# Kernel optimization log

Hardware: AMD Instinct MI355X
Metric: run time of the kernel (lower is better)

## Reference

```python
import jax, jax.numpy as jnp
import numpy as np

# tag2index constants
PAD, START, END, T = 0, 14, 15, 16
B, L, V, E, H = 128, 512, 30000, 256, 256


def _lstm(xs, w_ih, w_hh, b, reverse=False):
    """xs: [L, B, E] -> hs: [L, B, H]. PyTorch gate order i,f,g,o."""
    Bsz = xs.shape[1]
    Hd = w_hh.shape[1]
    def cell(carry, xt):
        h, c = carry
        g = xt @ w_ih.T + h @ w_hh.T + b  # [B, 4H]
        i, f, gg, o = jnp.split(g, 4, axis=-1)
        c = jax.nn.sigmoid(f) * c + jax.nn.sigmoid(i) * jnp.tanh(gg)
        h = jax.nn.sigmoid(o) * jnp.tanh(c)
        return (h, c), h
    init = (jnp.zeros((Bsz, Hd), xs.dtype), jnp.zeros((Bsz, Hd), xs.dtype))
    _, hs = jax.lax.scan(cell, init, xs, reverse=reverse)
    return hs


def setup_inputs() -> dict:
    key = jax.random.key(0)
    ks = jax.random.split(key, 12)
    batch_data = jax.random.randint(ks[0], (B, L), 0, V, dtype=jnp.int32)
    # variable-length tags with contiguous trailing PAD (as the model assumes)
    lengths = jax.random.randint(ks[1], (B,), L // 4, L + 1)
    raw_tags = jax.random.randint(ks[2], (B, L), 1, 14, dtype=jnp.int32)  # real tags in [1,14)
    pos = jnp.arange(L)[None, :]
    batch_tag = jnp.where(pos < lengths[:, None], raw_tags, PAD).astype(jnp.int32)
    s = 0.05
    emb = jax.random.normal(ks[3], (V, E), jnp.float32) * s
    w_ih_f = jax.random.normal(ks[4], (4 * H, E), jnp.float32) * s
    w_hh_f = jax.random.normal(ks[5], (4 * H, H), jnp.float32) * s
    b_f = jnp.zeros((4 * H,), jnp.float32)
    w_ih_b = jax.random.normal(ks[6], (4 * H, E), jnp.float32) * s
    w_hh_b = jax.random.normal(ks[7], (4 * H, H), jnp.float32) * s
    b_b = jnp.zeros((4 * H,), jnp.float32)
    w_cls = jax.random.normal(ks[8], (T, 2 * H), jnp.float32) * s
    b_cls = jnp.zeros((T,), jnp.float32)
    transition = jnp.full((T, T), 1.0 / T, jnp.float32)
    return {"batch_data": batch_data, "batch_tag": batch_tag, "emb": emb,
            "w_ih_f": w_ih_f, "w_hh_f": w_hh_f, "b_f": b_f,
            "w_ih_b": w_ih_b, "w_hh_b": w_hh_b, "b_b": b_b,
            "w_cls": w_cls, "b_cls": b_cls, "transition": transition}


def reference(batch_data, batch_tag, emb, w_ih_f, w_hh_f, b_f,
              w_ih_b, w_hh_b, b_b, w_cls, b_cls, transition):
    # ---- BiLSTM encoder ----
    x = emb[batch_data]                      # [B, L, E]
    xs = jnp.moveaxis(x, 1, 0)               # [L, B, E]
    hf = _lstm(xs, w_ih_f, w_hh_f, b_f, reverse=False)
    hb = _lstm(xs, w_ih_b, w_hh_b, b_b, reverse=True)
    out = jnp.moveaxis(jnp.concatenate([hf, hb], axis=-1), 0, 1)  # [B, L, 2H]
    emission = out @ w_cls.T + b_cls          # [B, L, T]
    crf_scores = emission[:, :, None, :] + transition[None, None]  # [B, L, T, T]

    # ---- CRF loss (linear-chain forward algorithm) ----
    mask = batch_tag != PAD                   # [B, L]
    lengths = mask.sum(axis=1)                # [B]
    prev = jnp.concatenate(
        [jnp.full((B, 1), START, batch_tag.dtype), batch_tag[:, :-1]], axis=1)
    idx = (batch_tag + prev * T).astype(jnp.int32)  # flat (prev_tag, cur_tag) index
    flat = crf_scores.reshape(B, L, T * T)
    g = jnp.take_along_axis(flat, idx[:, :, None], axis=2)[..., 0]
    golden_scores = jnp.sum(jnp.where(mask, g, 0.0))

    sc_t = jnp.moveaxis(crf_scores, 1, 0)     # [L, B, T, T]
    init = sc_t[0, :, START, :]               # [B, T] (all lengths >= 1)
    def step(prev_scores, x_t):
        sc, t = x_t
        new = jax.nn.logsumexp(sc + prev_scores[:, :, None], axis=1)  # [B, T]
        active = (lengths > t)[:, None]
        return jnp.where(active, new, prev_scores), None
    final, _ = jax.lax.scan(step, init, (sc_t[1:], jnp.arange(1, L)))
    all_path_scores = jnp.sum(final[:, END])
    loss = (all_path_scores - golden_scores) / B
    return loss
```

## Files before the change

kernel.cpp:

```cpp
#include <hip/hip_runtime.h>

#define Bsz 128
#define Lseq 512
#define Hdim 256
#define Tn 16
#define START_TAG 14
#define END_TAG 15

typedef float f32x4 __attribute__((ext_vector_type(4)));
typedef short s16x8 __attribute__((ext_vector_type(8)));

__device__ __forceinline__ unsigned short f2bf(float f) {
    unsigned int u = __builtin_bit_cast(unsigned int, f);
    u += 0x7fffu + ((u >> 16) & 1u);
    return (unsigned short)(u >> 16);
}
__device__ __forceinline__ float bf2f(unsigned int bits16) {
    return __builtin_bit_cast(float, bits16 << 16);
}
__device__ __forceinline__ float sigmoidf_(float x) {
    return 1.0f / (1.0f + __expf(-x));
}

__global__ void embprep_kernel(const float* __restrict__ emb,
                               unsigned int* __restrict__ embb, int n2) {
    int i = blockIdx.x * blockDim.x + threadIdx.x;
    int stride = gridDim.x * blockDim.x;
    for (; i < n2; i += stride)
        embb[i] = (unsigned int)f2bf(emb[2 * i]) | ((unsigned int)f2bf(emb[2 * i + 1]) << 16);
}

__global__ void wprep_kernel(const float* __restrict__ wih_f, const float* __restrict__ whh_f,
                             const float* __restrict__ wih_b, const float* __restrict__ whh_b,
                             unsigned int* __restrict__ wtile) {
    int bid = blockIdx.x;
    int ki  = bid & 15;
    int wv  = (bid >> 4) & 3;
    int ug  = (bid >> 6) & 15;
    int dir = bid >> 10;
    int t = threadIdx.x;
    int lane = t >> 2, j = t & 3;
    int n = lane & 15, kq = lane >> 4;
    int k0 = ki * 32 + kq * 8 + 2 * j;
    int col = (n & 3) * 256 + ug * 16 + wv * 4 + (n >> 2);
    const float* wih = dir ? wih_b : wih_f;
    const float* whh = dir ? whh_b : whh_f;
    float f0, f1;
    if (k0 < 256) { f0 = wih[col * 256 + k0];       f1 = wih[col * 256 + k0 + 1]; }
    else          { f0 = whh[col * 256 + k0 - 256]; f1 = whh[col * 256 + k0 - 255]; }
    wtile[(size_t)bid * 256 + t] = (unsigned int)f2bf(f0) | ((unsigned int)f2bf(f1) << 16);
}

__global__ void lengths_kernel(const int* __restrict__ tag, int* __restrict__ lengths) {
    int b = blockIdx.x;
    int tid = threadIdx.x;
    int cnt = 0;
    for (int l = tid; l < Lseq; l += blockDim.x)
        cnt += (tag[b * Lseq + l] != 0) ? 1 : 0;
    for (int off = 32; off > 0; off >>= 1) cnt += __shfl_down(cnt, off);
    __shared__ int red[4];
    if ((tid & 63) == 0) red[tid >> 6] = cnt;
    __syncthreads();
    if (tid == 0) lengths[b] = red[0] + red[1] + red[2] + red[3];
}

__global__ __launch_bounds__(256, 1) void bilstm_persist(
    const int* __restrict__ bd,
    const unsigned int* __restrict__ embb,
    const unsigned int* __restrict__ wtile,
    const float* __restrict__ b_f, const float* __restrict__ b_b,
    const float* __restrict__ w_cls,
    float* __restrict__ em_f, float* __restrict__ em_b,
    unsigned int* __restrict__ ring)
{
    const int wg  = blockIdx.x;
    const int dir = wg >> 7;
    const int bg  = (wg >> 4) & 7;
    const int ug  = wg & 15;
    const int tid = threadIdx.x;
    const int gb0 = bg * 16;

    __shared__ unsigned int h_lds[2][16 * 132];
    __shared__ float wcls_lds[256];

    wcls_lds[tid] = w_cls[(size_t)ug * (2 * Hdim) + dir * Hdim + tid];

    const int wv = tid >> 6;
    const int l  = tid & 63;
    const int n  = l & 15;
    const int kq = l >> 4;

    uint4 w_reg[16];
    {
        const unsigned int* wsrc =
            wtile + ((size_t)((dir * 16 + ug) * 4 + wv) * 16) * 256 + l * 4;
        #pragma unroll
        for (int ki = 0; ki < 16; ++ki)
            w_reg[ki] = *(const uint4*)(wsrc + ki * 256);
    }
    const float bias_lane = (dir ? b_b : b_f)[(n & 3) * 256 + ug * 16 + wv * 4 + (n >> 2)];
    float c_reg[4] = {0.f, 0.f, 0.f, 0.f};
    const int* bdr = bd + (size_t)(gb0 + n) * Lseq;
    unsigned int* rb = ring + (size_t)dir * 2 * 16384;
    const bool storer = ((l & 7) == 0);
    const int store_col = ug * 8 + wv * 2 + ((n >> 2) >> 1);
    float* emout = dir ? em_b : em_f;

    const int pm = tid >> 4, pq0 = (tid & 15) * 8;

    __syncthreads();

    f32x4 acc_x = {0.f, 0.f, 0.f, 0.f};
    {
        const int t0 = dir ? (Lseq - 1) : 0;
        int tok = bdr[t0];
        const unsigned int* xsrc = embb + (size_t)tok * 128 + kq * 4;
        #pragma unroll
        for (int ki = 0; ki < 8; ++ki) {
            s16x8 a = __builtin_bit_cast(s16x8, *(const uint4*)(xsrc + ki * 16));
            acc_x = __builtin_amdgcn_mfma_f32_16x16x32_bf16(
                a, __builtin_bit_cast(s16x8, w_reg[ki]), acc_x, 0, 0, 0);
        }
    }

    for (int s = 0; s < Lseq; ++s) {
        {
            const unsigned int* src = rb + ((s + 1) & 1) * 16384 + (gb0 + pm) * 128 + pq0;
            const unsigned int want = (((s + 3) >> 1) & 1) * 0x00010001u;
            unsigned int v[8];
            #pragma unroll
            for (int j = 0; j < 8; ++j)
                v[j] = __hip_atomic_load(src + j, __ATOMIC_RELAXED, __HIP_MEMORY_SCOPE_AGENT);
            bool again = true;
            while (again) {
                again = false;
                #pragma unroll
                for (int j = 0; j < 8; ++j)
                    if ((v[j] & 0x00010001u) != want) {
                        v[j] = __hip_atomic_load(src + j, __ATOMIC_RELAXED,
                                                 __HIP_MEMORY_SCOPE_AGENT);
                        again = true;
                    }
            }
            unsigned int* dst = &h_lds[s & 1][pm * 132 + pq0];
            *(uint4*)dst       = make_uint4(v[0], v[1], v[2], v[3]);
            *(uint4*)(dst + 4) = make_uint4(v[4], v[5], v[6], v[7]);
        }
        __syncthreads();
        const unsigned int* hb = &h_lds[s & 1][0];

        if (wv == 0 && s > 0) {
            float p = 0.f;
            #pragma unroll
            for (int kih = 0; kih < 8; ++kih) {
                const unsigned int* hp = &hb[n * 132 + kih * 16 + kq * 4];
                const float* wc = &wcls_lds[kih * 32 + kq * 8];
                #pragma unroll
                for (int j = 0; j < 4; ++j) {
                    unsigned int v = hp[j];
                    p += bf2f(v & 0xffffu) * wc[2 * j] + bf2f(v >> 16) * wc[2 * j + 1];
                }
            }
            p += __shfl_xor(p, 16);
            p += __shfl_xor(p, 32);
            if (l < 16) {
                int t_prev = dir ? (Lseq - s) : (s - 1);
                emout[((size_t)(gb0 + l) * Lseq + t_prev) * Tn + ug] = p;
            }
        }

        f32x4 acc = acc_x;
        #pragma unroll
        for (int kih = 0; kih < 8; ++kih) {
            s16x8 a = *(const s16x8*)&hb[n * 132 + kih * 16 + kq * 4];
            acc = __builtin_amdgcn_mfma_f32_16x16x32_bf16(
                a, __builtin_bit_cast(s16x8, w_reg[8 + kih]), acc, 0, 0, 0);
        }

        {
            const unsigned int ep = (unsigned int)((s >> 1) & 1);
            const int base = l & ~3;
            unsigned int hbits[4];
            #pragma unroll
            for (int r = 0; r < 4; ++r) {
                float pre = acc[r] + bias_lane;
                float gi = __shfl(pre, base);
                float gf = __shfl(pre, base + 1);
                float gg = __shfl(pre, base + 2);
                float go = __shfl(pre, base + 3);
                float cn = sigmoidf_(gf) * c_reg[r] + sigmoidf_(gi) * tanhf(gg);
                c_reg[r] = cn;
                float hn = sigmoidf_(go) * tanhf(cn);
                hbits[r] = ((unsigned int)f2bf(hn) & 0xFFFEu) | ep;
            }
            unsigned int* dstrow = rb + (s & 1) * 16384;
            #pragma unroll
            for (int r = 0; r < 4; ++r) {
                unsigned int partner = (unsigned int)__shfl((int)hbits[r], l + 4);
                if (storer) {
                    unsigned int pk = hbits[r] | (partner << 16);
                    __hip_atomic_store(dstrow + (gb0 + kq * 4 + r) * 128 + store_col, pk,
                                       __ATOMIC_RELAXED, __HIP_MEMORY_SCOPE_AGENT);
                }
            }
        }

        if (s + 1 < Lseq) {
            const int tn = dir ? (Lseq - 2 - s) : (s + 1);
            int tok = bdr[tn];
            const unsigned int* xsrc = embb + (size_t)tok * 128 + kq * 4;
            f32x4 ax = {0.f, 0.f, 0.f, 0.f};
            #pragma unroll
            for (int ki = 0; ki < 8; ++ki) {
                s16x8 a = __builtin_bit_cast(s16x8, *(const uint4*)(xsrc + ki * 16));
                ax = __builtin_amdgcn_mfma_f32_16x16x32_bf16(
                    a, __builtin_bit_cast(s16x8, w_reg[ki]), ax, 0, 0, 0);
            }
            acc_x = ax;
        }
    }

    {
        const int s = Lseq;
        const unsigned int* src = rb + ((s + 1) & 1) * 16384 + (gb0 + pm) * 128 + pq0;
        const unsigned int want = (((s + 3) >> 1) & 1) * 0x00010001u;
        unsigned int v[8];
        #pragma unroll
        for (int j = 0; j < 8; ++j)
            v[j] = __hip_atomic_load(src + j, __ATOMIC_RELAXED, __HIP_MEMORY_SCOPE_AGENT);
        bool again = true;
        while (again) {
            again = false;
            #pragma unroll
            for (int j = 0; j < 8; ++j)
                if ((v[j] & 0x00010001u) != want) {
                    v[j] = __hip_atomic_load(src + j, __ATOMIC_RELAXED,
                                             __HIP_MEMORY_SCOPE_AGENT);
                    again = true;
                }
        }
        unsigned int* dst = &h_lds[0][pm * 132 + pq0];
        *(uint4*)dst       = make_uint4(v[0], v[1], v[2], v[3]);
        *(uint4*)(dst + 4) = make_uint4(v[4], v[5], v[6], v[7]);
        __syncthreads();
        if (wv == 0) {
            const unsigned int* hb = &h_lds[0][0];
            float p = 0.f;
            #pragma unroll
            for (int kih = 0; kih < 8; ++kih) {
                const unsigned int* hp = &hb[n * 132 + kih * 16 + kq * 4];
                const float* wc = &wcls_lds[kih * 32 + kq * 8];
                #pragma unroll
                for (int j = 0; j < 4; ++j) {
                    unsigned int vv = hp[j];
                    p += bf2f(vv & 0xffffu) * wc[2 * j] + bf2f(vv >> 16) * wc[2 * j + 1];
                }
            }
            p += __shfl_xor(p, 16);
            p += __shfl_xor(p, 32);
            if (l < 16) {
                int t_tail = dir ? 0 : (Lseq - 1);
                emout[((size_t)(gb0 + l) * Lseq + t_tail) * Tn + ug] = p;
            }
        }
    }
}

__global__ void golden_kernel(const int* __restrict__ tag,
                              const float* __restrict__ em_f,
                              const float* __restrict__ em_b,
                              const float* __restrict__ b_cls,
                              const float* __restrict__ trans,
                              float* __restrict__ golden)
{
    int b = blockIdx.x;
    int tid = threadIdx.x;
    float s = 0.f;
    for (int l = tid; l < Lseq; l += blockDim.x) {
        int tg = tag[b * Lseq + l];
        if (tg != 0) {
            int prev = (l == 0) ? START_TAG : tag[b * Lseq + l - 1];
            size_t e = ((size_t)b * Lseq + l) * Tn + tg;
            s += em_f[e] + em_b[e] + b_cls[tg] + trans[prev * Tn + tg];
        }
    }
    for (int off = 32; off > 0; off >>= 1) s += __shfl_down(s, off);
    __shared__ float red[4];
    if ((tid & 63) == 0) red[tid >> 6] = s;
    __syncthreads();
    if (tid == 0) atomicAdd(golden, red[0] + red[1] + red[2] + red[3]);
}

__global__ void crf_forward_kernel(const float* __restrict__ em_f,
                                   const float* __restrict__ em_b,
                                   const float* __restrict__ b_cls,
                                   const float* __restrict__ trans,
                                   const int* __restrict__ lengths,
                                   float* __restrict__ allpath)
{
    int b = blockIdx.x;
    int lane = threadIdx.x;
    int j = lane & 15;
    float tcol[16];
    #pragma unroll
    for (int i = 0; i < 16; ++i) tcol[i] = trans[i * Tn + j];
    float bc = b_cls[j];
    size_t e0 = ((size_t)b * Lseq) * Tn + j;
    float alpha = em_f[e0] + em_b[e0] + bc + tcol[START_TAG];
    int len = lengths[b];
    for (int t = 1; t < Lseq; ++t) {
        float av[16];
        float m = -1e30f;
        #pragma unroll
        for (int i = 0; i < 16; ++i) {
            av[i] = __shfl(alpha, i) + tcol[i];
            m = fmaxf(m, av[i]);
        }
        float sum = 0.f;
        #pragma unroll
        for (int i = 0; i < 16; ++i) sum += __expf(av[i] - m);
        size_t e = ((size_t)b * Lseq + t) * Tn + j;
        float nv = em_f[e] + em_b[e] + bc + m + __logf(sum);
        alpha = (t < len) ? nv : alpha;
    }
    if (lane == END_TAG) atomicAdd(allpath, alpha);
}

__global__ void finalize_kernel(const float* __restrict__ scal, float* __restrict__ out) {
    out[0] = (scal[1] - scal[0]) / (float)Bsz;
}

extern "C" void kernel_launch(void* const* d_in, const int* in_sizes, int n_in,
                              void* d_out, int out_size, void* d_ws, size_t ws_size,
                              hipStream_t stream)
{
    (void)in_sizes; (void)n_in; (void)out_size; (void)ws_size;
    const int*   bd     = (const int*)d_in[0];
    const int*   tag    = (const int*)d_in[1];
    const float* emb    = (const float*)d_in[2];
    const float* w_ih_f = (const float*)d_in[3];
    const float* w_hh_f = (const float*)d_in[4];
    const float* b_f    = (const float*)d_in[5];
    const float* w_ih_b = (const float*)d_in[6];
    const float* w_hh_b = (const float*)d_in[7];
    const float* b_b    = (const float*)d_in[8];
    const float* w_cls  = (const float*)d_in[9];
    const float* b_cls  = (const float*)d_in[10];
    const float* trans  = (const float*)d_in[11];
    float* out = (float*)d_out;

    float* ws = (float*)d_ws;
    float* em_f = ws;
    float* em_b = em_f + (size_t)Bsz * Lseq * Tn;
    unsigned int* ring = (unsigned int*)(em_b + (size_t)Bsz * Lseq * Tn);
    float* scal = (float*)(ring + 65536);
    int* lengths = (int*)(scal + 8);
    unsigned int* wtile = (unsigned int*)(lengths + 128);
    unsigned int* embb = wtile + (size_t)524288;

    hipMemsetAsync(ring, 0x01, (size_t)65536 * 4, stream);
    hipMemsetAsync(scal, 0, 8 * sizeof(float), stream);

    embprep_kernel<<<2048, 256, 0, stream>>>(emb, embb, 30000 * 128);
    wprep_kernel<<<2048, 256, 0, stream>>>(w_ih_f, w_hh_f, w_ih_b, w_hh_b, wtile);
    lengths_kernel<<<Bsz, 256, 0, stream>>>(tag, lengths);

    void* kargs[] = {
        (void*)&bd, (void*)&embb, (void*)&wtile,
        (void*)&b_f, (void*)&b_b, (void*)&w_cls,
        (void*)&em_f, (void*)&em_b, (void*)&ring
    };
    hipLaunchCooperativeKernel((const void*)bilstm_persist,
                               dim3(256), dim3(256), kargs, 0, stream);

    golden_kernel<<<Bsz, 256, 0, stream>>>(tag, em_f, em_b, b_cls, trans, scal);
    crf_forward_kernel<<<Bsz, 64, 0, stream>>>(em_f, em_b, b_cls, trans, lengths, scal + 1);
    finalize_kernel<<<1, 1, 0, stream>>>(scal, out);
}
```

Baseline: 2.678 ms.

## Add per-wave step flags, reorganize h ring layout, spread emission projection across waves

Adds a per-group flag array that each wave bumps after storing its h slice; consumers spin on these flags with a wave-wide vote before polling the data ring. The ring is relaid out so each unit-group writes a contiguous 1024-word slab, and the LDS row stride is padded to 148 words to cut bank conflicts. The x-embedding loads are issued early, before the recurrent MFMA, so their latency overlaps it. The classifier projection of h now runs on all four waves after the recurrent step rather than on wave 0 before it, taking it off the critical path. The cost is an extra flag write and poll per step, which adds global atomic traffic on the serial recurrence.

```diff
diff --git a/kernel.cpp b/kernel.cpp
--- a/kernel.cpp
+++ b/kernel.cpp
@@ -6,6 +6,7 @@
 #define Tn 16
 #define START_TAG 14
 #define END_TAG 15
+#define HSTRIDE 148
 
 typedef float f32x4 __attribute__((ext_vector_type(4)));
 typedef short s16x8 __attribute__((ext_vector_type(8)));
@@ -71,16 +72,18 @@
     const float* __restrict__ b_f, const float* __restrict__ b_b,
     const float* __restrict__ w_cls,
     float* __restrict__ em_f, float* __restrict__ em_b,
-    unsigned int* __restrict__ ring)
+    unsigned int* __restrict__ ring,
+    int* __restrict__ flags)
 {
     const int wg  = blockIdx.x;
     const int dir = wg >> 7;
     const int bg  = (wg >> 4) & 7;
     const int ug  = wg & 15;
+    const int grp = dir * 8 + bg;
     const int tid = threadIdx.x;
     const int gb0 = bg * 16;
 
-    __shared__ unsigned int h_lds[2][16 * 132];
+    __shared__ unsigned int h_lds[2][16 * HSTRIDE];
     __shared__ float wcls_lds[256];
 
     wcls_lds[tid] = w_cls[(size_t)ug * (2 * Hdim) + dir * Hdim + tid];
@@ -101,12 +104,16 @@
     const float bias_lane = (dir ? b_b : b_f)[(n & 3) * 256 + ug * 16 + wv * 4 + (n >> 2)];
     float c_reg[4] = {0.f, 0.f, 0.f, 0.f};
     const int* bdr = bd + (size_t)(gb0 + n) * Lseq;
-    unsigned int* rb = ring + (size_t)dir * 2 * 16384;
+    unsigned int* rb = ring + (size_t)dir * 32768;
+    int* flg = &flags[grp * 64];
     const bool storer = ((l & 7) == 0);
-    const int store_col = ug * 8 + wv * 2 + ((n >> 2) >> 1);
+    const int store_off = wv * 2 + (n >> 3);
     float* emout = dir ? em_b : em_f;
 
-    const int pm = tid >> 4, pq0 = (tid & 15) * 8;
+    const int sc = tid & 15, sm = tid >> 4;
+
+    const int batch_e = wv * 4 + (kq);
+    const int kseg = n;
 
     __syncthreads();
 
@@ -124,8 +131,15 @@
     }
 
     for (int s = 0; s < Lseq; ++s) {
+        if (s > 0) {
+            while (true) {
+                int v = __hip_atomic_load(&flg[l], __ATOMIC_RELAXED, __HIP_MEMORY_SCOPE_AGENT);
+                if (__all(v >= s)) break;
+            }
+        }
+
         {
-            const unsigned int* src = rb + ((s + 1) & 1) * 16384 + (gb0 + pm) * 128 + pq0;
+            const unsigned int* src = rb + ((s + 1) & 1) * 16384 + sc * 1024 + (gb0 + sm) * 8;
             const unsigned int want = (((s + 3) >> 1) & 1) * 0x00010001u;
             unsigned int v[8];
             #pragma unroll
@@ -142,37 +156,28 @@
                         again = true;
                     }
             }
-            unsigned int* dst = &h_lds[s & 1][pm * 132 + pq0];
+            unsigned int* dst = &h_lds[s & 1][sm * HSTRIDE + sc * 8];
             *(uint4*)dst       = make_uint4(v[0], v[1], v[2], v[3]);
             *(uint4*)(dst + 4) = make_uint4(v[4], v[5], v[6], v[7]);
         }
         __syncthreads();
         const unsigned int* hb = &h_lds[s & 1][0];
 
-        if (wv == 0 && s > 0) {
-            float p = 0.f;
-            #pragma unroll
-            for (int kih = 0; kih < 8; ++kih) {
-                const unsigned int* hp = &hb[n * 132 + kih * 16 + kq * 4];
-                const float* wc = &wcls_lds[kih * 32 + kq * 8];
-                #pragma unroll
-                for (int j = 0; j < 4; ++j) {
-                    unsigned int v = hp[j];
-                    p += bf2f(v & 0xffffu) * wc[2 * j] + bf2f(v >> 16) * wc[2 * j + 1];
-                }
-            }
-            p += __shfl_xor(p, 16);
-            p += __shfl_xor(p, 32);
-            if (l < 16) {
-                int t_prev = dir ? (Lseq - s) : (s - 1);
-                emout[((size_t)(gb0 + l) * Lseq + t_prev) * Tn + ug] = p;
-            }
+        uint4 xf[8];
+        const bool havex = (s + 1 < Lseq);
+        if (havex) {
+            const int tn = dir ? (Lseq - 2 - s) : (s + 1);
+            int tok = bdr[tn];
+            const unsigned int* xsrc = embb + (size_t)tok * 128 + kq * 4;
+            #pragma unroll
+            for (int ki = 0; ki < 8; ++ki)
+                xf[ki] = *(const uint4*)(xsrc + ki * 16);
         }
 
         f32x4 acc = acc_x;
         #pragma unroll
         for (int kih = 0; kih < 8; ++kih) {
-            s16x8 a = *(const s16x8*)&hb[n * 132 + kih * 16 + kq * 4];
+            s16x8 a = *(const s16x8*)&hb[n * HSTRIDE + kih * 16 + kq * 4];
             acc = __builtin_amdgcn_mfma_f32_16x16x32_bf16(
                 a, __builtin_bit_cast(s16x8, w_reg[8 + kih]), acc, 0, 0, 0);
         }
@@ -193,36 +198,58 @@
                 float hn = sigmoidf_(go) * tanhf(cn);
                 hbits[r] = ((unsigned int)f2bf(hn) & 0xFFFEu) | ep;
             }
-            unsigned int* dstrow = rb + (s & 1) * 16384;
+            unsigned int* dstrow = rb + (s & 1) * 16384 + ug * 1024;
             #pragma unroll
             for (int r = 0; r < 4; ++r) {
                 unsigned int partner = (unsigned int)__shfl((int)hbits[r], l + 4);
                 if (storer) {
                     unsigned int pk = hbits[r] | (partner << 16);
-                    __hip_atomic_store(dstrow + (gb0 + kq * 4 + r) * 128 + store_col, pk,
+                    __hip_atomic_store(dstrow + (gb0 + kq * 4 + r) * 8 + store_off, pk,
                                        __ATOMIC_RELAXED, __HIP_MEMORY_SCOPE_AGENT);
                 }
             }
         }
 
-        if (s + 1 < Lseq) {
-            const int tn = dir ? (Lseq - 2 - s) : (s + 1);
-            int tok = bdr[tn];
-            const unsigned int* xsrc = embb + (size_t)tok * 128 + kq * 4;
+        if (l == 0)
+            __hip_atomic_store(&flg[ug * 4 + wv], s + 1,
+                               __ATOMIC_RELAXED, __HIP_MEMORY_SCOPE_AGENT);
+
+        if (havex) {
             f32x4 ax = {0.f, 0.f, 0.f, 0.f};
             #pragma unroll
             for (int ki = 0; ki < 8; ++ki) {
-                s16x8 a = __builtin_bit_cast(s16x8, *(const uint4*)(xsrc + ki * 16));
                 ax = __builtin_amdgcn_mfma_f32_16x16x32_bf16(
-                    a, __builtin_bit_cast(s16x8, w_reg[ki]), ax, 0, 0, 0);
+                    __builtin_bit_cast(s16x8, xf[ki]),
+                    __builtin_bit_cast(s16x8, w_reg[ki]), ax, 0, 0, 0);
             }
             acc_x = ax;
+        }
+
+        if (s > 0) {
+            const unsigned int* hr = &hb[batch_e * HSTRIDE + kseg * 8];
+            float p = 0.f;
+            #pragma unroll
+            for (int j = 0; j < 8; ++j) {
+                unsigned int v = hr[j];
+                int k0 = kseg * 16 + 2 * j;
+                p += bf2f(v & 0xffffu) * wcls_lds[k0] + bf2f(v >> 16) * wcls_lds[k0 + 1];
+            }
+            #pragma unroll
+            for (int m = 1; m < 16; m <<= 1) p += __shfl_xor(p, m);
+            if (n == 0) {
+                int t_prev = dir ? (Lseq - s) : (s - 1);
+                emout[((size_t)(gb0 + batch_e) * Lseq + t_prev) * Tn + ug] = p;
+            }
         }
     }
 
     {
         const int s = Lseq;
-        const unsigned int* src = rb + ((s + 1) & 1) * 16384 + (gb0 + pm) * 128 + pq0;
+        while (true) {
+            int v = __hip_atomic_load(&flg[l], __ATOMIC_RELAXED, __HIP_MEMORY_SCOPE_AGENT);
+            if (__all(v >= s)) break;
+        }
+        const unsigned int* src = rb + ((s + 1) & 1) * 16384 + sc * 1024 + (gb0 + sm) * 8;
         const unsigned int want = (((s + 3) >> 1) & 1) * 0x00010001u;
         unsigned int v[8];
         #pragma unroll
@@ -239,28 +266,25 @@
                     again = true;
                 }
         }
-        unsigned int* dst = &h_lds[0][pm * 132 + pq0];
+        unsigned int* dst = &h_lds[s & 1][sm * HSTRIDE + sc * 8];
         *(uint4*)dst       = make_uint4(v[0], v[1], v[2], v[3]);
         *(uint4*)(dst + 4) = make_uint4(v[4], v[5], v[6], v[7]);
         __syncthreads();
-        if (wv == 0) {
-            const unsigned int* hb = &h_lds[0][0];
+        const unsigned int* hb = &h_lds[s & 1][0];
+        {
+            const unsigned int* hr = &hb[batch_e * HSTRIDE + kseg * 8];
             float p = 0.f;
             #pragma unroll
-            for (int kih = 0; kih < 8; ++kih) {
-                const unsigned int* hp = &hb[n * 132 + kih * 16 + kq * 4];
-                const float* wc = &wcls_lds[kih * 32 + kq * 8];
-                #pragma unroll
-                for (int j = 0; j < 4; ++j) {
-                    unsigned int vv = hp[j];
-                    p += bf2f(vv & 0xffffu) * wc[2 * j] + bf2f(vv >> 16) * wc[2 * j + 1];
-                }
-            }
-            p += __shfl_xor(p, 16);
-            p += __shfl_xor(p, 32);
-            if (l < 16) {
+            for (int j = 0; j < 8; ++j) {
+                unsigned int vv = hr[j];
+                int k0 = kseg * 16 + 2 * j;
+                p += bf2f(vv & 0xffffu) * wcls_lds[k0] + bf2f(vv >> 16) * wcls_lds[k0 + 1];
+            }
+            #pragma unroll
+            for (int m = 1; m < 16; m <<= 1) p += __shfl_xor(p, m);
+            if (n == 0) {
                 int t_tail = dir ? 0 : (Lseq - 1);
-                emout[((size_t)(gb0 + l) * Lseq + t_tail) * Tn + ug] = p;
+                emout[((size_t)(gb0 + batch_e) * Lseq + t_tail) * Tn + ug] = p;
             }
         }
     }
@@ -354,12 +378,13 @@
     float* em_b = em_f + (size_t)Bsz * Lseq * Tn;
     unsigned int* ring = (unsigned int*)(em_b + (size_t)Bsz * Lseq * Tn);
     float* scal = (float*)(ring + 65536);
-    int* lengths = (int*)(scal + 8);
+    int* flags = (int*)(scal + 8);
+    int* lengths = flags + 1024;
     unsigned int* wtile = (unsigned int*)(lengths + 128);
     unsigned int* embb = wtile + (size_t)524288;
 
     hipMemsetAsync(ring, 0x01, (size_t)65536 * 4, stream);
-    hipMemsetAsync(scal, 0, 8 * sizeof(float), stream);
+    hipMemsetAsync(scal, 0, (8 + 1024) * sizeof(float), stream);
 
     embprep_kernel<<<2048, 256, 0, stream>>>(emb, embb, 30000 * 128);
     wprep_kernel<<<2048, 256, 0, stream>>>(w_ih_f, w_hh_f, w_ih_b, w_hh_b, wtile);
@@ -368,7 +393,7 @@
     void* kargs[] = {
         (void*)&bd, (void*)&embb, (void*)&wtile,
         (void*)&b_f, (void*)&b_b, (void*)&w_cls,
-        (void*)&em_f, (void*)&em_b, (void*)&ring
+        (void*)&em_f, (void*)&em_b, (void*)&ring, (void*)&flags
     };
     hipLaunchCooperativeKernel((const void*)bilstm_persist,
                                dim3(256), dim3(256), kargs, 0, stream);
```

Result: slower. 2.928 ms (+9.3%).

## Restructure persistent BiLSTM into 64 larger workgroups with split input/recurrent warps

Applied to the files above, without the earlier changes.

The persistent LSTM kernel moves from 256 workgroups of 256 threads to 64 workgroups of 512 threads. Each workgroup covers 64 hidden units for one batch group, so cross-workgroup mailbox exchange is confined to 4 workgroups per batch group instead of a global ring. Warps are specialized: four compute the next step's input projection (with bias folded in) into a double-buffered LDS buffer and the emission projection via MFMA with bf16 classifier weights, while four run the recurrent MFMA and gate math. This cuts the number of synchronizing workgroups and moves input projection off the critical path, in exchange for higher register pressure (32 uint4 weight registers per thread), an extra prep kernel, and bf16 rounding of the classifier weights.

```diff
diff --git a/kernel.cpp b/kernel.cpp
--- a/kernel.cpp
+++ b/kernel.cpp
@@ -10,10 +10,10 @@
 typedef float f32x4 __attribute__((ext_vector_type(4)));
 typedef short s16x8 __attribute__((ext_vector_type(8)));
 
-__device__ __forceinline__ unsigned short f2bf(float f) {
+__device__ __forceinline__ unsigned int f2bf(float f) {
     unsigned int u = __builtin_bit_cast(unsigned int, f);
     u += 0x7fffu + ((u >> 16) & 1u);
-    return (unsigned short)(u >> 16);
+    return u >> 16;
 }
 __device__ __forceinline__ float bf2f(unsigned int bits16) {
     return __builtin_bit_cast(float, bits16 << 16);
@@ -27,28 +27,41 @@
     int i = blockIdx.x * blockDim.x + threadIdx.x;
     int stride = gridDim.x * blockDim.x;
     for (; i < n2; i += stride)
-        embb[i] = (unsigned int)f2bf(emb[2 * i]) | ((unsigned int)f2bf(emb[2 * i + 1]) << 16);
+        embb[i] = f2bf(emb[2 * i]) | (f2bf(emb[2 * i + 1]) << 16);
 }
 
 __global__ void wprep_kernel(const float* __restrict__ wih_f, const float* __restrict__ whh_f,
                              const float* __restrict__ wih_b, const float* __restrict__ whh_b,
                              unsigned int* __restrict__ wtile) {
-    int bid = blockIdx.x;
-    int ki  = bid & 15;
-    int wv  = (bid >> 4) & 3;
-    int ug  = (bid >> 6) & 15;
-    int dir = bid >> 10;
-    int t = threadIdx.x;
-    int lane = t >> 2, j = t & 3;
+    int flat = blockIdx.x * 256 + threadIdx.x;
+    int j    = flat & 3;
+    int lane = (flat >> 2) & 63;
+    int ks   = (flat >> 8) & 7;
+    int tt   = (flat >> 11) & 3;
+    int wv   = (flat >> 13) & 7;
+    int q    = (flat >> 16) & 3;
+    int dir  = flat >> 18;
+    int p    = wv & 3;
     int n = lane & 15, kq = lane >> 4;
-    int k0 = ki * 32 + kq * 8 + 2 * j;
-    int col = (n & 3) * 256 + ug * 16 + wv * 4 + (n >> 2);
-    const float* wih = dir ? wih_b : wih_f;
-    const float* whh = dir ? whh_b : whh_f;
-    float f0, f1;
-    if (k0 < 256) { f0 = wih[col * 256 + k0];       f1 = wih[col * 256 + k0 + 1]; }
-    else          { f0 = whh[col * 256 + k0 - 256]; f1 = whh[col * 256 + k0 - 255]; }
-    wtile[(size_t)bid * 256 + t] = (unsigned int)f2bf(f0) | ((unsigned int)f2bf(f1) << 16);
+    int col = (n & 3) * 256 + q * 64 + (p * 4 + tt) * 4 + (n >> 2);
+    int k0 = ks * 32 + kq * 8 + 2 * j;
+    const float* w = (wv < 4) ? (dir ? wih_b : wih_f) : (dir ? whh_b : whh_f);
+    float f0 = w[col * 256 + k0], f1 = w[col * 256 + k0 + 1];
+    wtile[flat] = f2bf(f0) | (f2bf(f1) << 16);
+}
+
+__global__ void wclsprep_kernel(const float* __restrict__ w_cls,
+                                unsigned int* __restrict__ wclsb) {
+    int flat = blockIdx.x * 256 + threadIdx.x;
+    int j    = flat & 3;
+    int lane = (flat >> 2) & 63;
+    int ks   = (flat >> 8) & 7;
+    int dir  = flat >> 11;
+    int n = lane & 15, kq = lane >> 4;
+    int k0 = ks * 32 + kq * 8 + 2 * j;
+    float f0 = w_cls[n * 512 + dir * 256 + k0];
+    float f1 = w_cls[n * 512 + dir * 256 + k0 + 1];
+    wclsb[flat] = f2bf(f0) | (f2bf(f1) << 16);
 }
 
 __global__ void lengths_kernel(const int* __restrict__ tag, int* __restrict__ lengths) {
@@ -64,204 +77,216 @@
     if (tid == 0) lengths[b] = red[0] + red[1] + red[2] + red[3];
 }
 
-__global__ __launch_bounds__(256, 1) void bilstm_persist(
+__global__ __launch_bounds__(512, 2) void bilstm_persist(
     const int* __restrict__ bd,
     const unsigned int* __restrict__ embb,
     const unsigned int* __restrict__ wtile,
+    const unsigned int* __restrict__ wclsb,
     const float* __restrict__ b_f, const float* __restrict__ b_b,
-    const float* __restrict__ w_cls,
     float* __restrict__ em_f, float* __restrict__ em_b,
-    unsigned int* __restrict__ ring)
+    unsigned int* __restrict__ mbox)
 {
     const int wg  = blockIdx.x;
-    const int dir = wg >> 7;
-    const int bg  = (wg >> 4) & 7;
-    const int ug  = wg & 15;
+    const int dir = wg >> 5;
+    const int bg  = (wg >> 2) & 7;
+    const int q   = wg & 3;
     const int tid = threadIdx.x;
     const int gb0 = bg * 16;
 
     __shared__ unsigned int h_lds[2][16 * 132];
-    __shared__ float wcls_lds[256];
-
-    wcls_lds[tid] = w_cls[(size_t)ug * (2 * Hdim) + dir * Hdim + tid];
+    __shared__ f32x4 xp[2][16 * 64];
 
     const int wv = tid >> 6;
     const int l  = tid & 63;
     const int n  = l & 15;
     const int kq = l >> 4;
-
-    uint4 w_reg[16];
+    const bool is_h = (wv >= 4);
+    const int p  = wv & 3;
+
+    uint4 w_reg[4][8];
     {
         const unsigned int* wsrc =
-            wtile + ((size_t)((dir * 16 + ug) * 4 + wv) * 16) * 256 + l * 4;
-        #pragma unroll
-        for (int ki = 0; ki < 16; ++ki)
-            w_reg[ki] = *(const uint4*)(wsrc + ki * 256);
-    }
-    const float bias_lane = (dir ? b_b : b_f)[(n & 3) * 256 + ug * 16 + wv * 4 + (n >> 2)];
+            wtile + ((size_t)((dir * 4 + q) * 8 + wv)) * 8192 + l * 4;
+        #pragma unroll
+        for (int tt = 0; tt < 4; ++tt)
+            #pragma unroll
+            for (int ks = 0; ks < 8; ++ks)
+                w_reg[tt][ks] = *(const uint4*)(wsrc + (tt * 8 + ks) * 256);
+    }
+    float breg[4];
+    {
+        const float* bias = dir ? b_b : b_f;
+        #pragma unroll
+        for (int tt = 0; tt < 4; ++tt)
+            breg[tt] = bias[(n & 3) * 256 + q * 64 + (p * 4 + tt) * 4 + (n >> 2)];
+    }
+    uint4 wcls_reg[8];
+    if (!is_h && p == 0) {
+        const unsigned int* ws = wclsb + (size_t)dir * 2048 + l * 4;
+        #pragma unroll
+        for (int ks = 0; ks < 8; ++ks)
+            wcls_reg[ks] = *(const uint4*)(ws + ks * 256);
+    }
+
     float c_reg[4] = {0.f, 0.f, 0.f, 0.f};
     const int* bdr = bd + (size_t)(gb0 + n) * Lseq;
-    unsigned int* rb = ring + (size_t)dir * 2 * 16384;
-    const bool storer = ((l & 7) == 0);
-    const int store_col = ug * 8 + wv * 2 + ((n >> 2) >> 1);
+    unsigned int* mb = mbox + (size_t)(dir * 8 + bg) * 2 * 2048;
     float* emout = dir ? em_b : em_f;
 
-    const int pm = tid >> 4, pq0 = (tid & 15) * 8;
-
-    __syncthreads();
-
-    f32x4 acc_x = {0.f, 0.f, 0.f, 0.f};
-    {
+    const int pb = tid >> 5, pc = tid & 31;
+
+    if (!is_h) {
         const int t0 = dir ? (Lseq - 1) : 0;
         int tok = bdr[t0];
         const unsigned int* xsrc = embb + (size_t)tok * 128 + kq * 4;
-        #pragma unroll
-        for (int ki = 0; ki < 8; ++ki) {
-            s16x8 a = __builtin_bit_cast(s16x8, *(const uint4*)(xsrc + ki * 16));
-            acc_x = __builtin_amdgcn_mfma_f32_16x16x32_bf16(
-                a, __builtin_bit_cast(s16x8, w_reg[ki]), acc_x, 0, 0, 0);
-        }
+        f32x4 acc[4];
+        #pragma unroll
+        for (int tt = 0; tt < 4; ++tt) acc[tt] = {breg[tt], breg[tt], breg[tt], breg[tt]};
+        #pragma unroll
+        for (int ks = 0; ks < 8; ++ks) {
+            s16x8 a = __builtin_bit_cast(s16x8, *(const uint4*)(xsrc + ks * 16));
+            #pragma unroll
+            for (int tt = 0; tt < 4; ++tt)
+                acc[tt] = __builtin_amdgcn_mfma_f32_16x16x32_bf16(
+                    a, __builtin_bit_cast(s16x8, w_reg[tt][ks]), acc[tt], 0, 0, 0);
+        }
+        #pragma unroll
+        for (int tt = 0; tt < 4; ++tt) xp[0][(p * 4 + tt) * 64 + l] = acc[tt];
     }
 
     for (int s = 0; s < Lseq; ++s) {
         {
-            const unsigned int* src = rb + ((s + 1) & 1) * 16384 + (gb0 + pm) * 128 + pq0;
+            const unsigned int* src = mb + ((s + 1) & 1) * 2048 + pb * 128 + pc * 4;
             const unsigned int want = (((s + 3) >> 1) & 1) * 0x00010001u;
-            unsigned int v[8];
-            #pragma unroll
-            for (int j = 0; j < 8; ++j)
-                v[j] = __hip_atomic_load(src + j, __ATOMIC_RELAXED, __HIP_MEMORY_SCOPE_AGENT);
-            bool again = true;
-            while (again) {
-                again = false;
-                #pragma unroll
-                for (int j = 0; j < 8; ++j)
-                    if ((v[j] & 0x00010001u) != want) {
-                        v[j] = __hip_atomic_load(src + j, __ATOMIC_RELAXED,
-                                                 __HIP_MEMORY_SCOPE_AGENT);
-                        again = true;
-                    }
-            }
-            unsigned int* dst = &h_lds[s & 1][pm * 132 + pq0];
-            *(uint4*)dst       = make_uint4(v[0], v[1], v[2], v[3]);
-            *(uint4*)(dst + 4) = make_uint4(v[4], v[5], v[6], v[7]);
+            unsigned int v0, v1, v2, v3;
+            v0 = __hip_atomic_load(src + 0, __ATOMIC_RELAXED, __HIP_MEMORY_SCOPE_AGENT);
+            v1 = __hip_atomic_load(src + 1, __ATOMIC_RELAXED, __HIP_MEMORY_SCOPE_AGENT);
+            v2 = __hip_atomic_load(src + 2, __ATOMIC_RELAXED, __HIP_MEMORY_SCOPE_AGENT);
+            v3 = __hip_atomic_load(src + 3, __ATOMIC_RELAXED, __HIP_MEMORY_SCOPE_AGENT);
+            while (((v0 & 0x00010001u) != want) | ((v1 & 0x00010001u) != want) |
+                   ((v2 & 0x00010001u) != want) | ((v3 & 0x00010001u) != want)) {
+                __builtin_amdgcn_s_sleep(1);
+                v0 = __hip_atomic_load(src + 0, __ATOMIC_RELAXED, __HIP_MEMORY_SCOPE_AGENT);
+                v1 = __hip_atomic_load(src + 1, __ATOMIC_RELAXED, __HIP_MEMORY_SCOPE_AGENT);
+                v2 = __hip_atomic_load(src + 2, __ATOMIC_RELAXED, __HIP_MEMORY_SCOPE_AGENT);
+                v3 = __hip_atomic_load(src + 3, __ATOMIC_RELAXED, __HIP_MEMORY_SCOPE_AGENT);
+            }
+            *(uint4*)&h_lds[s & 1][pb * 132 + pc * 4] = make_uint4(v0, v1, v2, v3);
         }
         __syncthreads();
-        const unsigned int* hb = &h_lds[s & 1][0];
-
-        if (wv == 0 && s > 0) {
-            float p = 0.f;
-            #pragma unroll
-            for (int kih = 0; kih < 8; ++kih) {
-                const unsigned int* hp = &hb[n * 132 + kih * 16 + kq * 4];
-                const float* wc = &wcls_lds[kih * 32 + kq * 8];
-                #pragma unroll
-                for (int j = 0; j < 4; ++j) {
-                    unsigned int v = hp[j];
-                    p += bf2f(v & 0xffffu) * wc[2 * j] + bf2f(v >> 16) * wc[2 * j + 1];
-                }
-            }
-            p += __shfl_xor(p, 16);
-            p += __shfl_xor(p, 32);
-            if (l < 16) {
-                int t_prev = dir ? (Lseq - s) : (s - 1);
-                emout[((size_t)(gb0 + l) * Lseq + t_prev) * Tn + ug] = p;
-            }
-        }
-
-        f32x4 acc = acc_x;
-        #pragma unroll
-        for (int kih = 0; kih < 8; ++kih) {
-            s16x8 a = *(const s16x8*)&hb[n * 132 + kih * 16 + kq * 4];
-            acc = __builtin_amdgcn_mfma_f32_16x16x32_bf16(
-                a, __builtin_bit_cast(s16x8, w_reg[8 + kih]), acc, 0, 0, 0);
-        }
-
-        {
+
+        if (is_h) {
+            f32x4 acc[4];
+            #pragma unroll
+            for (int tt = 0; tt < 4; ++tt) acc[tt] = xp[s & 1][(p * 4 + tt) * 64 + l];
+            #pragma unroll
+            for (int ks = 0; ks < 8; ++ks) {
+                s16x8 a = *(const s16x8*)&h_lds[s & 1][n * 132 + ks * 16 + kq * 4];
+                #pragma unroll
+                for (int tt = 0; tt < 4; ++tt)
+                    acc[tt] = __builtin_amdgcn_mfma_f32_16x16x32_bf16(
+                        a, __builtin_bit_cast(s16x8, w_reg[tt][ks]), acc[tt], 0, 0, 0);
+            }
             const unsigned int ep = (unsigned int)((s >> 1) & 1);
             const int base = l & ~3;
-            unsigned int hbits[4];
-            #pragma unroll
-            for (int r = 0; r < 4; ++r) {
-                float pre = acc[r] + bias_lane;
-                float gi = __shfl(pre, base);
-                float gf = __shfl(pre, base + 1);
-                float gg = __shfl(pre, base + 2);
-                float go = __shfl(pre, base + 3);
-                float cn = sigmoidf_(gf) * c_reg[r] + sigmoidf_(gi) * tanhf(gg);
-                c_reg[r] = cn;
+            const int rsel = n & 3;
+            unsigned int* slot = mb + (s & 1) * 2048;
+            #pragma unroll
+            for (int tt = 0; tt < 4; ++tt) {
+                float p0 = acc[tt][0], p1 = acc[tt][1], p2 = acc[tt][2], p3 = acc[tt][3];
+                float a0, a1, a2, a3, gi, gf, gg, go;
+                a0 = __shfl(p0, base);     a1 = __shfl(p1, base);
+                a2 = __shfl(p2, base);     a3 = __shfl(p3, base);
+                gi = (rsel == 0) ? a0 : (rsel == 1) ? a1 : (rsel == 2) ? a2 : a3;
+                a0 = __shfl(p0, base + 1); a1 = __shfl(p1, base + 1);
+                a2 = __shfl(p2, base + 1); a3 = __shfl(p3, base + 1);
+                gf = (rsel == 0) ? a0 : (rsel == 1) ? a1 : (rsel == 2) ? a2 : a3;
+                a0 = __shfl(p0, base + 2); a1 = __shfl(p1, base + 2);
+                a2 = __shfl(p2, base + 2); a3 = __shfl(p3, base + 2);
+                gg = (rsel == 0) ? a0 : (rsel == 1) ? a1 : (rsel == 2) ? a2 : a3;
+                a0 = __shfl(p0, base + 3); a1 = __shfl(p1, base + 3);
+                a2 = __shfl(p2, base + 3); a3 = __shfl(p3, base + 3);
+                go = (rsel == 0) ? a0 : (rsel == 1) ? a1 : (rsel == 2) ? a2 : a3;
+                float cn = sigmoidf_(gf) * c_reg[tt] + sigmoidf_(gi) * tanhf(gg);
+                c_reg[tt] = cn;
                 float hn = sigmoidf_(go) * tanhf(cn);
-                hbits[r] = ((unsigned int)f2bf(hn) & 0xFFFEu) | ep;
-            }
-            unsigned int* dstrow = rb + (s & 1) * 16384;
-            #pragma unroll
-            for (int r = 0; r < 4; ++r) {
-                unsigned int partner = (unsigned int)__shfl((int)hbits[r], l + 4);
-                if (storer) {
-                    unsigned int pk = hbits[r] | (partner << 16);
-                    __hip_atomic_store(dstrow + (gb0 + kq * 4 + r) * 128 + store_col, pk,
+                unsigned int hb16 = (f2bf(hn) & 0xFFFEu) | ep;
+                unsigned int partner = (unsigned int)__shfl((int)hb16, l + 4);
+                if ((n & 4) == 0) {
+                    int b = kq * 4 + rsel;
+                    int uidx = q * 32 + p * 8 + tt * 2 + (n >> 3);
+                    __hip_atomic_store(slot + b * 128 + uidx, hb16 | (partner << 16),
                                        __ATOMIC_RELAXED, __HIP_MEMORY_SCOPE_AGENT);
                 }
             }
-        }
-
-        if (s + 1 < Lseq) {
-            const int tn = dir ? (Lseq - 2 - s) : (s + 1);
-            int tok = bdr[tn];
-            const unsigned int* xsrc = embb + (size_t)tok * 128 + kq * 4;
-            f32x4 ax = {0.f, 0.f, 0.f, 0.f};
-            #pragma unroll
-            for (int ki = 0; ki < 8; ++ki) {
-                s16x8 a = __builtin_bit_cast(s16x8, *(const uint4*)(xsrc + ki * 16));
-                ax = __builtin_amdgcn_mfma_f32_16x16x32_bf16(
-                    a, __builtin_bit_cast(s16x8, w_reg[ki]), ax, 0, 0, 0);
-            }
-            acc_x = ax;
+        } else {
+            if (s + 1 < Lseq) {
+                const int tn = dir ? (Lseq - 2 - s) : (s + 1);
+                int tok = bdr[tn];
+                const unsigned int* xsrc = embb + (size_t)tok * 128 + kq * 4;
+                f32x4 acc[4];
+                #pragma unroll
+                for (int tt = 0; tt < 4; ++tt)
+                    acc[tt] = {breg[tt], breg[tt], breg[tt], breg[tt]};
+                #pragma unroll
+                for (int ks = 0; ks < 8; ++ks) {
+                    s16x8 a = __builtin_bit_cast(s16x8, *(const uint4*)(xsrc + ks * 16));
+                    #pragma unroll
+                    for (int tt = 0; tt < 4; ++tt)
+                        acc[tt] = __builtin_amdgcn_mfma_f32_16x16x32_bf16(
+                            a, __builtin_bit_cast(s16x8, w_reg[tt][ks]), acc[tt], 0, 0, 0);
+                }
+                #pragma unroll
+                for (int tt = 0; tt < 4; ++tt)
+                    xp[(s + 1) & 1][(p * 4 + tt) * 64 + l] = acc[tt];
+            }
+            if (p == 0 && s > 0) {
+                f32x4 eacc = {0.f, 0.f, 0.f, 0.f};
+                #pragma unroll
+                for (int ks = 0; ks < 8; ++ks) {
+                    s16x8 a = *(const s16x8*)&h_lds[s & 1][n * 132 + ks * 16 + kq * 4];
+                    eacc = __builtin_amdgcn_mfma_f32_16x16x32_bf16(
+                        a, __builtin_bit_cast(s16x8, wcls_reg[ks]), eacc, 0, 0, 0);
+                }
+                int t_prev = dir ? (Lseq - s) : (s - 1);
+                #pragma unroll
+                for (int r = 0; r < 4; ++r)
+                    emout[((size_t)(gb0 + kq * 4 + r) * Lseq + t_prev) * Tn + n] = eacc[r];
+            }
         }
     }
 
     {
         const int s = Lseq;
-        const unsigned int* src = rb + ((s + 1) & 1) * 16384 + (gb0 + pm) * 128 + pq0;
+        const unsigned int* src = mb + ((s + 1) & 1) * 2048 + pb * 128 + pc * 4;
         const unsigned int want = (((s + 3) >> 1) & 1) * 0x00010001u;
-        unsigned int v[8];
-        #pragma unroll
-        for (int j = 0; j < 8; ++j)
-            v[j] = __hip_atomic_load(src + j, __ATOMIC_RELAXED, __HIP_MEMORY_SCOPE_AGENT);
-        bool again = true;
-        while (again) {
-            again = false;
-            #pragma unroll
-            for (int j = 0; j < 8; ++j)
-                if ((v[j] & 0x00010001u) != want) {
-                    v[j] = __hip_atomic_load(src + j, __ATOMIC_RELAXED,
-                                             __HIP_MEMORY_SCOPE_AGENT);
-                    again = true;
-                }
-        }
-        unsigned int* dst = &h_lds[0][pm * 132 + pq0];
-        *(uint4*)dst       = make_uint4(v[0], v[1], v[2], v[3]);
-        *(uint4*)(dst + 4) = make_uint4(v[4], v[5], v[6], v[7]);
+        unsigned int v0, v1, v2, v3;
+        v0 = __hip_atomic_load(src + 0, __ATOMIC_RELAXED, __HIP_MEMORY_SCOPE_AGENT);
+        v1 = __hip_atomic_load(src + 1, __ATOMIC_RELAXED, __HIP_MEMORY_SCOPE_AGENT);
+        v2 = __hip_atomic_load(src + 2, __ATOMIC_RELAXED, __HIP_MEMORY_SCOPE_AGENT);
+        v3 = __hip_atomic_load(src + 3, __ATOMIC_RELAXED, __HIP_MEMORY_SCOPE_AGENT);
+        while (((v0 & 0x00010001u) != want) | ((v1 & 0x00010001u) != want) |
+               ((v2 & 0x00010001u) != want) | ((v3 & 0x00010001u) != want)) {
+            __builtin_amdgcn_s_sleep(1);
+            v0 = __hip_atomic_load(src + 0, __ATOMIC_RELAXED, __HIP_MEMORY_SCOPE_AGENT);
+            v1 = __hip_atomic_load(src + 1, __ATOMIC_RELAXED, __HIP_MEMORY_SCOPE_AGENT);
+            v2 = __hip_atomic_load(src + 2, __ATOMIC_RELAXED, __HIP_MEMORY_SCOPE_AGENT);
+            v3 = __hip_atomic_load(src + 3, __ATOMIC_RELAXED, __HIP_MEMORY_SCOPE_AGENT);
+        }
+        *(uint4*)&h_lds[0][pb * 132 + pc * 4] = make_uint4(v0, v1, v2, v3);
         __syncthreads();
-        if (wv == 0) {
-            const unsigned int* hb = &h_lds[0][0];
-            float p = 0.f;
-            #pragma unroll
-            for (int kih = 0; kih < 8; ++kih) {
-                const unsigned int* hp = &hb[n * 132 + kih * 16 + kq * 4];
-                const float* wc = &wcls_lds[kih * 32 + kq * 8];
-                #pragma unroll
-                for (int j = 0; j < 4; ++j) {
-                    unsigned int vv = hp[j];
-                    p += bf2f(vv & 0xffffu) * wc[2 * j] + bf2f(vv >> 16) * wc[2 * j + 1];
-                }
-            }
-            p += __shfl_xor(p, 16);
-            p += __shfl_xor(p, 32);
-            if (l < 16) {
-                int t_tail = dir ? 0 : (Lseq - 1);
-                emout[((size_t)(gb0 + l) * Lseq + t_tail) * Tn + ug] = p;
-            }
+        if (!is_h && p == 0) {
+            f32x4 eacc = {0.f, 0.f, 0.f, 0.f};
+            #pragma unroll
+            for (int ks = 0; ks < 8; ++ks) {
+                s16x8 a = *(const s16x8*)&h_lds[0][n * 132 + ks * 16 + kq * 4];
+                eacc = __builtin_amdgcn_mfma_f32_16x16x32_bf16(
+                    a, __builtin_bit_cast(s16x8, wcls_reg[ks]), eacc, 0, 0, 0);
+            }
+            int t_tail = dir ? 0 : (Lseq - 1);
+            #pragma unroll
+            for (int r = 0; r < 4; ++r)
+                emout[((size_t)(gb0 + kq * 4 + r) * Lseq + t_tail) * Tn + n] = eacc[r];
         }
     }
 }
@@ -352,26 +377,28 @@
     float* ws = (float*)d_ws;
     float* em_f = ws;
     float* em_b = em_f + (size_t)Bsz * Lseq * Tn;
-    unsigned int* ring = (unsigned int*)(em_b + (size_t)Bsz * Lseq * Tn);
-    float* scal = (float*)(ring + 65536);
+    unsigned int* mbox = (unsigned int*)(em_b + (size_t)Bsz * Lseq * Tn);
+    float* scal = (float*)(mbox + 65536);
     int* lengths = (int*)(scal + 8);
     unsigned int* wtile = (unsigned int*)(lengths + 128);
-    unsigned int* embb = wtile + (size_t)524288;
-
-    hipMemsetAsync(ring, 0x01, (size_t)65536 * 4, stream);
+    unsigned int* wclsb = wtile + 524288;
+    unsigned int* embb  = wclsb + 4096;
+
+    hipMemsetAsync(mbox, 0x01, (size_t)65536 * 4, stream);
     hipMemsetAsync(scal, 0, 8 * sizeof(float), stream);
 
     embprep_kernel<<<2048, 256, 0, stream>>>(emb, embb, 30000 * 128);
     wprep_kernel<<<2048, 256, 0, stream>>>(w_ih_f, w_hh_f, w_ih_b, w_hh_b, wtile);
+    wclsprep_kernel<<<16, 256, 0, stream>>>(w_cls, wclsb);
     lengths_kernel<<<Bsz, 256, 0, stream>>>(tag, lengths);
 
     void* kargs[] = {
-        (void*)&bd, (void*)&embb, (void*)&wtile,
-        (void*)&b_f, (void*)&b_b, (void*)&w_cls,
-        (void*)&em_f, (void*)&em_b, (void*)&ring
+        (void*)&bd, (void*)&embb, (void*)&wtile, (void*)&wclsb,
+        (void*)&b_f, (void*)&b_b,
+        (void*)&em_f, (void*)&em_b, (void*)&mbox
     };
     hipLaunchCooperativeKernel((const void*)bilstm_persist,
-                               dim3(256), dim3(256), kargs, 0, stream);
+                               dim3(64), dim3(512), kargs, 0, stream);
 
     golden_kernel<<<Bsz, 256, 0, stream>>>(tag, em_f, em_b, b_cls, trans, scal);
     crf_forward_kernel<<<Bsz, 64, 0, stream>>>(em_f, em_b, b_cls, trans, lengths, scal + 1);
```

After: 2.413 ms. -9.9%, faster.
